# Kernel tuning notes

Hardware: AMD Instinct MI355X
Metric: run time of the kernel (lower is better)

The kernel has to match this reference:

```python
import jax, jax.numpy as jnp
import numpy as np

THRESHOLD = 0.3

def setup_inputs() -> dict:
    key = jax.random.key(0)
    ks = jax.random.split(key, 8)
    B, T, N, d = 4, 32, 1024, 2
    hd, od, hs, osz = 64, 64, 128, 2
    p = lambda k, sh: jax.random.normal(k, sh, jnp.float32) * 0.1
    return {
        "points": jax.random.uniform(ks[0], (B, T, N, d), jnp.float32),
        "W1": p(ks[1], (hd, d)),   "b1": jnp.zeros((hd,), jnp.float32),
        "W2": p(ks[2], (od, hd)),  "b2": jnp.zeros((od,), jnp.float32),
        "Wg": p(ks[3], (hd, od)),  "bg": jnp.zeros((hd,), jnp.float32),
        "Wih": p(ks[4], (3 * hs, hd)), "Whh": p(ks[5], (3 * hs, hs)),
        "bih": jnp.zeros((3 * hs,), jnp.float32), "bhh": jnp.zeros((3 * hs,), jnp.float32),
        "Wf": p(ks[6], (osz, hs)), "bf": jnp.zeros((osz,), jnp.float32),
    }

def _gcn_step(pts, W1, b1, W2, b2, Wg, bg):
    # pts: [N, d]. Torch detaches node features & adjacency (no grad to points).
    pts = jax.lax.stop_gradient(pts)
    dist = jnp.linalg.norm(pts[:, None, :] - pts[None, :, :], axis=2)  # [N,N]
    A = (dist < THRESHOLD).astype(pts.dtype)
    dinv = 1.0 / jnp.sqrt(A.sum(axis=1))          # rowsum >= 1 (self-loop)
    An = A * dinv[:, None] * dinv[None, :]        # D^{-1/2} A D^{-1/2}
    x = jax.nn.relu((An @ pts) @ W1.T + b1)       # [N, hd]
    x = jax.nn.relu((An @ x) @ W2.T + b2)         # [N, od]
    return x.mean(axis=0) @ Wg.T + bg             # [hd]

def reference(points, W1, b1, W2, b2, Wg, bg, Wih, Whh, bih, bhh, Wf, bf):
    # GCN per (batch, time): [B, T, hd]
    gcn = jax.vmap(jax.vmap(lambda p: _gcn_step(p, W1, b1, W2, b2, Wg, bg)))(points)
    H = Whh.shape[1]

    def gru_step(h, x):  # torch GRU gate order: r, z, n
        gi = x @ Wih.T + bih
        gh = h @ Whh.T + bhh
        ir, iz, inn = jnp.split(gi, 3)
        hr, hz, hn = jnp.split(gh, 3)
        r = jax.nn.sigmoid(ir + hr)
        z = jax.nn.sigmoid(iz + hz)
        n = jnp.tanh(inn + r * hn)
        h_new = (1.0 - z) * n + z * h
        return h_new, h_new

    h0 = jnp.zeros((H,), points.dtype)
    run = lambda xs: jax.lax.scan(gru_step, h0, xs)[1]   # [T, H]
    hs = jax.vmap(run)(gcn)                              # [B, T, H]
    y = hs @ Wf.T + bf                                   # [B, T, out]
    # torch: per-element gru_out.mean(dim=1, keepdim=True) on [1,T,out] -> [1,1,out], stacked -> [B,1,1,out]
    return y.mean(axis=1, keepdims=True)[:, :, None, :]
```

## Files before the change

kernel.cpp:

```cpp
#include <hip/hip_runtime.h>
#include <hip/hip_bf16.h>
#include <math.h>

#define N_PTS 1024
#define BT    128
typedef unsigned int u32;
typedef __attribute__((ext_vector_type(8))) short short8_t;
typedef __attribute__((ext_vector_type(4))) float f32x4;

__device__ __forceinline__ float bfi(u32 bits16) {
    union { u32 u; float f; } v; v.u = bits16 << 16; return v.f;
}
__device__ __forceinline__ unsigned short f2bf(float f) {
    union { float f; u32 u; } v; v.f = f;
    return (unsigned short)((v.u + 0x7FFFu + ((v.u >> 16) & 1u)) >> 16);
}
__device__ __forceinline__ float ldf(const void* p, int i, bool bf) {
    return bf ? bfi(((const unsigned short*)p)[i]) : ((const float*)p)[i];
}
__device__ __forceinline__ float2 ldp(const void* pbase, int j, bool bf) {
    if (bf) {
        u32 w = ((const u32*)pbase)[j];
        return make_float2(bfi(w & 0xFFFFu), bfi(w >> 16));
    }
    return ((const float2*)pbase)[j];
}
__device__ __forceinline__ bool detect_bf16(const void* pts, int tid, int* s_flag) {
    if (tid < 64) {
        u32 w = ((const u32*)pts)[tid];
        float v = bfi(w & 0xFFFFu);
        bool ok = (v >= 0.0f) && (v <= 1.0f);
        unsigned long long m = __ballot(ok);
        if (tid == 0) *s_flag = (m == 0xFFFFFFFFFFFFFFFFull) ? 1 : 0;
    }
    __syncthreads();
    return *s_flag != 0;
}
__device__ __forceinline__ bool is_nb(float px, float py, float qx, float qy) {
    float dx = px - qx, dy = py - qy;
    float d2 = __fadd_rn(__fmul_rn(dx, dx), __fmul_rn(dy, dy));
    return d2 < 0.09f;
}
__device__ __forceinline__ const void* pts_base(const void* pts, int bt, bool bf) {
    return bf ? (const void*)((const unsigned short*)pts + (size_t)bt * N_PTS * 2)
              : (const void*)((const float*)pts + (size_t)bt * N_PTS * 2);
}
__device__ __forceinline__ void gload16(const u32* g, u32* l) {
    __builtin_amdgcn_global_load_lds((const __attribute__((address_space(1))) u32*)g,
                                     (__attribute__((address_space(3))) u32*)l, 16, 0, 0);
}
__device__ __forceinline__ float rdlane(float v, int i) {
    return __int_as_float(__builtin_amdgcn_readlane(__float_as_int(v), i));
}
__device__ __forceinline__ float sigm_f(float x) {
    return __fdividef(1.0f, 1.0f + __expf(-x));
}
__device__ __forceinline__ float tanh_f(float x) {
    float e = __expf(2.0f * x);
    return 1.0f - __fdividef(2.0f, e + 1.0f);
}

__global__ __launch_bounds__(256) void k1_bm(const void* __restrict__ pts,
                                             float* __restrict__ dinv,
                                             float* __restrict__ gsum,
                                             u32* __restrict__ bm) {
    int blk = blockIdx.x, tid = threadIdx.x;
    int bt = blk >> 2, q = blk & 3;
    __shared__ float2 sp[N_PTS];
    __shared__ int s_flag;
    bool bf = detect_bf16(pts, tid, &s_flag);
    const void* pb = pts_base(pts, bt, bf);
    for (int j = tid; j < N_PTS; j += 256) sp[j] = ldp(pb, j, bf);
    if (blk < 32) gsum[blk * 256 + tid] = 0.0f;
    __syncthreads();
    int i = q * 256 + tid;
    float px = sp[i].x, py = sp[i].y;
    const float4* sp4 = (const float4*)sp;
    u32* bmrow = bm + (size_t)bt * 32768 + i;
    int cnt = 0;
    for (int c = 0; c < 32; c++) {
        u32 m = 0;
#pragma unroll
        for (int h = 0; h < 8; h++) {
            float4 s01 = sp4[c * 16 + 2 * h], s23 = sp4[c * 16 + 2 * h + 1];
            if (is_nb(px, py, s01.x, s01.y)) m |= 1u << (4 * h);
            if (is_nb(px, py, s01.z, s01.w)) m |= 1u << (4 * h + 1);
            if (is_nb(px, py, s23.x, s23.y)) m |= 1u << (4 * h + 2);
            if (is_nb(px, py, s23.z, s23.w)) m |= 1u << (4 * h + 3);
        }
        bmrow[c * 1024] = m;
        cnt += __popc(m);
    }
    dinv[bt * N_PTS + i] = 1.0f / sqrtf((float)cnt);
}

__global__ __launch_bounds__(256) void k2_x1v(const void* __restrict__ pts,
                                              const void* __restrict__ W1,
                                              const void* __restrict__ b1,
                                              const float* __restrict__ dinv,
                                              const u32* __restrict__ bm,
                                              u32* __restrict__ x1vB) {
    int blk = blockIdx.x, tid = threadIdx.x;
    int bt = blk >> 2, q = blk & 3;
    __shared__ float2 sud[N_PTS];
    __shared__ float2 sax[256];
    __shared__ float  sdl[256];
    __shared__ int s_flag;
    bool bf = detect_bf16(pts, tid, &s_flag);
    const void* pb = pts_base(pts, bt, bf);
    for (int j = tid; j < N_PTS; j += 256) {
        float2 p = ldp(pb, j, bf);
        float d = dinv[bt * N_PTS + j];
        sud[j] = make_float2(d * p.x, d * p.y);
    }
    __syncthreads();
    int i = q * 256 + tid;
    float ax = 0.f, ay = 0.f;
    const u32* bmr = bm + (size_t)bt * 32768 + i;
    for (int c = 0; c < 32; c++) {
        u32 m = bmr[c * 1024];
        const float4* uv = (const float4*)sud + c * 16;
#pragma unroll
        for (int h = 0; h < 16; h++) {
            float4 v = uv[h];
            bool b0 = (m >> (2 * h)) & 1u, b1_ = (m >> (2 * h + 1)) & 1u;
            ax += b0 ? v.x : 0.0f;  ay += b0 ? v.y : 0.0f;
            ax += b1_ ? v.z : 0.0f; ay += b1_ ? v.w : 0.0f;
        }
    }
    float di = dinv[bt * N_PTS + i];
    sax[tid] = make_float2(ax * di, ay * di);
    sdl[tid] = di;
    __syncthreads();
    int ch = tid & 63, wq = tid >> 6;
    float w0 = ldf(W1, 2 * ch, bf), w1v = ldf(W1, 2 * ch + 1, bf), bb = ldf(b1, ch, bf);
    for (int tt = 0; tt < 4; tt++) {
        u32 ow[8];
#pragma unroll
        for (int k2i = 0; k2i < 8; k2i++) {
            int lj = tt * 64 + wq * 16 + 2 * k2i;
            float2 a0 = sax[lj], a1 = sax[lj + 1];
            float v0 = sdl[lj]     * fmaxf(fmaf(w0, a0.x, fmaf(w1v, a0.y, bb)), 0.0f);
            float v1 = sdl[lj + 1] * fmaxf(fmaf(w0, a1.x, fmaf(w1v, a1.y, bb)), 0.0f);
            ow[k2i] = (u32)f2bf(v0) | ((u32)f2bf(v1) << 16);
        }
        u32* dst = x1vB + ((size_t)(bt * 16 + q * 4 + tt) * 64 + ch) * 36 + wq * 8;
        *(uint4*)dst = make_uint4(ow[0], ow[1], ow[2], ow[3]);
        *(uint4*)(dst + 4) = make_uint4(ow[4], ow[5], ow[6], ow[7]);
    }
}

__global__ __launch_bounds__(256) void k3_mfma(const void* __restrict__ pts,
                                               const void* __restrict__ W2,
                                               const void* __restrict__ b2,
                                               const float* __restrict__ dinv,
                                               const u32* __restrict__ bm,
                                               const u32* __restrict__ x1vB,
                                               float* __restrict__ gsum) {
    __shared__ u32 pool[15424];
    __shared__ int s_flag;
    float* poolf = (float*)pool;
    int tid = threadIdx.x, lane = tid & 63, w = tid >> 6;
    int l15 = lane & 15, quad = lane >> 4;
    int blk = blockIdx.x, bt = blk & 127, rowblk = blk >> 7;
    bool bf = detect_bf16(pts, tid, &s_flag);

    const u32* xg = x1vB + (size_t)bt * 36864;
    for (int it = w; it < 9; it += 4)
        gload16(xg + it * 256 + lane * 4, pool + 8192 + it * 256 + lane * 4);

    const u32* bg_ = bm + (size_t)bt * 32768 + rowblk * 256;
    for (int idx = tid; idx < 8192; idx += 256) {
        int c = idx >> 8, r = idx & 255;
        pool[idx] = bg_[c * 1024 + r];
    }
    unsigned short* W2B = (unsigned short*)(pool + 12800);
    for (int idx = tid; idx < 4096; idx += 256) {
        int o = idx >> 6, c = idx & 63;
        W2B[o * 72 + c] = f2bf(ldf(W2, idx, bf));
    }
    if (tid < 256) poolf[15104 + tid] = dinv[bt * N_PTS + rowblk * 256 + tid];
    if (tid < 64)  poolf[15360 + tid] = ldf(b2, tid, bf);

    f32x4 acc[4][4];
#pragma unroll
    for (int rf = 0; rf < 4; rf++)
#pragma unroll
        for (int nb = 0; nb < 4; nb++)
#pragma unroll
            for (int r = 0; r < 4; r++) acc[rf][nb][r] = 0.0f;

    for (int t = 0; t < 16; t++) {
        __syncthreads();
        if (t + 1 < 16) {
            u32* dst = pool + ((t & 1) ? 8192 : 10496);
            const u32* src = xg + (t + 1) * 2304;
            for (int it = w; it < 9; it += 4)
                gload16(src + it * 256 + lane * 4, dst + it * 256 + lane * 4);
        }
        const unsigned short* xf = (const unsigned short*)(pool + ((t & 1) ? 10496 : 8192));
#pragma unroll
        for (int ks = 0; ks < 2; ks++) {
            short8_t bq[4];
#pragma unroll
            for (int rf = 0; rf < 4; rf++) {
                u32 mw = pool[(2 * t + ks) * 256 + w * 64 + rf * 16 + l15];
                u32 by = (mw >> (quad * 8)) & 0xFFu;
                short8_t v;
#pragma unroll
                for (int i2 = 0; i2 < 8; i2++)
                    v[i2] = (by & (1u << i2)) ? (short)0x3F80 : (short)0;
                bq[rf] = v;
            }
#pragma unroll
            for (int nb = 0; nb < 4; nb++) {
                short8_t af = *(const short8_t*)(xf + (nb * 16 + l15) * 72 + ks * 32 + quad * 8);
#pragma unroll
                for (int rf = 0; rf < 4; rf++)
                    acc[rf][nb] = __builtin_amdgcn_mfma_f32_16x16x32_bf16(af, bq[rf], acc[rf][nb], 0, 0, 0);
            }
        }
    }
    __syncthreads();

    u32* dump = pool;
#pragma unroll
    for (int rf = 0; rf < 4; rf++) {
        int rn = w * 64 + rf * 16 + l15;
        float di = poolf[15104 + rn];
#pragma unroll
        for (int nb = 0; nb < 4; nb++) {
            u32 lo = (u32)f2bf(acc[rf][nb][0] * di) | ((u32)f2bf(acc[rf][nb][1] * di) << 16);
            u32 hi = (u32)f2bf(acc[rf][nb][2] * di) | ((u32)f2bf(acc[rf][nb][3] * di) << 16);
            u32* dst = dump + rn * 36 + nb * 8 + quad * 2;
            dst[0] = lo; dst[1] = hi;
        }
    }
    __syncthreads();
    f32x4 xacc[4][4];
#pragma unroll
    for (int ob = 0; ob < 4; ob++)
#pragma unroll
        for (int rf = 0; rf < 4; rf++)
#pragma unroll
            for (int r = 0; r < 4; r++) xacc[ob][rf][r] = 0.0f;
#pragma unroll
    for (int ks2 = 0; ks2 < 2; ks2++) {
        short8_t b2f[4];
#pragma unroll
        for (int rf = 0; rf < 4; rf++)
            b2f[rf] = *(const short8_t*)((const unsigned short*)dump +
                        (w * 64 + rf * 16 + l15) * 72 + ks2 * 32 + quad * 8);
#pragma unroll
        for (int ob = 0; ob < 4; ob++) {
            short8_t a2 = *(const short8_t*)(W2B + (ob * 16 + l15) * 72 + ks2 * 32 + quad * 8);
#pragma unroll
            for (int rf = 0; rf < 4; rf++)
                xacc[ob][rf] = __builtin_amdgcn_mfma_f32_16x16x32_bf16(a2, b2f[rf], xacc[ob][rf], 0, 0, 0);
        }
    }
#pragma unroll
    for (int ob = 0; ob < 4; ob++) {
#pragma unroll
        for (int r = 0; r < 4; r++) {
            int o = ob * 16 + quad * 4 + r;
            float bb = poolf[15360 + o];
            float s = 0.0f;
#pragma unroll
            for (int rf = 0; rf < 4; rf++) s += fmaxf(xacc[ob][rf][r] + bb, 0.0f);
            s += __shfl_down(s, 8, 16);
            s += __shfl_down(s, 4, 16);
            s += __shfl_down(s, 2, 16);
            s += __shfl_down(s, 1, 16);
            if (l15 == 0) atomicAdd(&gsum[bt * 64 + o], s);
        }
    }
}

__global__ __launch_bounds__(768, 1) void k4_all(const void* __restrict__ pts,
                                                 const void* __restrict__ Wg,
                                                 const void* __restrict__ bg,
                                                 const void* __restrict__ Wih,
                                                 const void* __restrict__ Whh,
                                                 const void* __restrict__ bih,
                                                 const void* __restrict__ bhh,
                                                 const void* __restrict__ Wf,
                                                 const void* __restrict__ bf_,
                                                 const float* __restrict__ gsum,
                                                 float* __restrict__ out) {
    int b = blockIdx.x, tid = threadIdx.x;
    __shared__ float s_gi[32 * 384];
    __shared__ float sWgT[64 * 65];
    __shared__ float s_gm[2048];
    __shared__ float s_x[2048];
    __shared__ float s_part[2][768];
    __shared__ float s_hm[128];
    __shared__ int s_flag;
    bool bf = detect_bf16(pts, tid, &s_flag);
    for (int idx = tid; idx < 4096; idx += 768) {
        int o = idx >> 6, k = idx & 63;
        sWgT[k * 65 + o] = ldf(Wg, idx, bf);
    }
    for (int idx = tid; idx < 2048; idx += 768)
        s_gm[idx] = gsum[(size_t)b * 2048 + idx] * (1.0f / 1024.0f);
    __syncthreads();
    for (int idx = tid; idx < 2048; idx += 768) {
        int t = idx >> 6, c = idx & 63;
        float s0 = ldf(bg, c, bf), s1 = 0.f, s2 = 0.f, s3 = 0.f;
        const float* gm = s_gm + t * 64;
#pragma unroll
        for (int k = 0; k < 64; k += 4) {
            s0 = fmaf(sWgT[k * 65 + c],       gm[k],     s0);
            s1 = fmaf(sWgT[(k + 1) * 65 + c], gm[k + 1], s1);
            s2 = fmaf(sWgT[(k + 2) * 65 + c], gm[k + 2], s2);
            s3 = fmaf(sWgT[(k + 3) * 65 + c], gm[k + 3], s3);
        }
        s_x[idx] = (s0 + s1) + (s2 + s3);
    }
    __syncthreads();
    int hi = (tid >= 384) ? 1 : 0;
    int r = tid - hi * 384;
    int lane = tid & 63;
    {
        float wv[64];
        if (bf) {
#pragma unroll
            for (int k = 0; k < 64; k++) wv[k] = bfi(((const unsigned short*)Wih)[r * 64 + k]);
        } else {
            const float4* wr = (const float4*)Wih + r * 16;
#pragma unroll
            for (int qq = 0; qq < 16; qq++) {
                float4 v = wr[qq];
                wv[4*qq] = v.x; wv[4*qq+1] = v.y; wv[4*qq+2] = v.z; wv[4*qq+3] = v.w;
            }
        }
        float br = ldf(bih, r, bf);
        for (int t = hi; t < 32; t += 2) {
            float xv = s_x[t * 64 + lane];
            float s0 = br, s1 = 0.f, s2 = 0.f, s3 = 0.f;
#pragma unroll
            for (int k = 0; k < 64; k += 4) {
                s0 = fmaf(wv[k],     rdlane(xv, k),     s0);
                s1 = fmaf(wv[k + 1], rdlane(xv, k + 1), s1);
                s2 = fmaf(wv[k + 2], rdlane(xv, k + 2), s2);
                s3 = fmaf(wv[k + 3], rdlane(xv, k + 3), s3);
            }
            s_gi[t * 384 + r] = (s0 + s1) + (s2 + s3);
        }
    }
    float wh2[64];
    {
        int koff = hi * 64;
        if (bf) {
#pragma unroll
            for (int k = 0; k < 64; k++)
                wh2[k] = bfi(((const unsigned short*)Whh)[r * 128 + koff + k]);
        } else {
            const float4* wr = (const float4*)Whh + (r * 128 + koff) / 4;
#pragma unroll
            for (int qq = 0; qq < 16; qq++) {
                float4 v = wr[qq];
                wh2[4*qq] = v.x; wh2[4*qq+1] = v.y; wh2[4*qq+2] = v.z; wh2[4*qq+3] = v.w;
            }
        }
    }
    float bhr = hi ? 0.0f : ldf(bhh, r, bf);
    int c = hi * 64 + lane;
    float hval = 0.0f;
    float hsum = 0.0f;
    __syncthreads();

    for (int t = 0; t < 32; t++) {
        float gi_r = s_gi[t * 384 + c];
        float gi_z = s_gi[t * 384 + 128 + c];
        float gi_n = s_gi[t * 384 + 256 + c];
        float s0 = bhr, s1 = 0.f, s2 = 0.f, s3 = 0.f;
#pragma unroll
        for (int k = 0; k < 64; k += 4) {
            s0 = fmaf(wh2[k],     rdlane(hval, k),     s0);
            s1 = fmaf(wh2[k + 1], rdlane(hval, k + 1), s1);
            s2 = fmaf(wh2[k + 2], rdlane(hval, k + 2), s2);
            s3 = fmaf(wh2[k + 3], rdlane(hval, k + 3), s3);
        }
        s_part[t & 1][tid] = (s0 + s1) + (s2 + s3);
        __syncthreads();
        const float* P = s_part[t & 1];
        float gr = gi_r + P[c]       + P[384 + c];
        float gz = gi_z + P[128 + c] + P[512 + c];
        float hn =        P[256 + c] + P[640 + c];
        float rr = sigm_f(gr);
        float z  = sigm_f(gz);
        float n  = tanh_f(fmaf(rr, hn, gi_n));
        hval = fmaf(z, hval - n, n);
        hsum += hval;
    }
    if (tid < 64) s_hm[tid] = hsum * (1.0f / 32.0f);
    else if (tid >= 384 && tid < 448) s_hm[64 + lane] = hsum * (1.0f / 32.0f);
    __syncthreads();
    if (tid < 128) {
        float hm = s_hm[tid];
        s_part[0][tid]       = ldf(Wf, tid, bf) * hm;
        s_part[0][128 + tid] = ldf(Wf, 128 + tid, bf) * hm;
    }
    __syncthreads();
    if (tid < 2) {
        float s = ldf(bf_, tid, bf);
        for (int k = 0; k < 128; k++) s += s_part[0][tid * 128 + k];
        out[b * 2 + tid] = s;
    }
}

extern "C" void kernel_launch(void* const* d_in, const int* in_sizes, int n_in,
                              void* d_out, int out_size, void* d_ws, size_t ws_size,
                              hipStream_t stream) {
    const void* pts = d_in[0];
    const void* W1  = d_in[1];
    const void* b1  = d_in[2];
    const void* W2  = d_in[3];
    const void* b2  = d_in[4];
    const void* Wg  = d_in[5];
    const void* bg  = d_in[6];
    const void* Wih = d_in[7];
    const void* Whh = d_in[8];
    const void* bih = d_in[9];
    const void* bhh = d_in[10];
    const void* Wf  = d_in[11];
    const void* bf_ = d_in[12];

    float* dinv = (float*)d_ws;
    float* gsum = dinv + (size_t)BT * N_PTS;
    u32*   bm   = (u32*)(gsum + BT * 64);
    u32*   x1vB = bm + (size_t)BT * 32768;

    k1_bm  <<<512, 256, 0, stream>>>(pts, dinv, gsum, bm);
    k2_x1v <<<512, 256, 0, stream>>>(pts, W1, b1, dinv, bm, x1vB);
    k3_mfma<<<512, 256, 0, stream>>>(pts, W2, b2, dinv, bm, x1vB, gsum);
    k4_all <<<4, 768, 0, stream>>>(pts, Wg, bg, Wih, Whh, bih, bhh, Wf, bf_,
                                   gsum, (float*)d_out);
}
```

Baseline: 242.2 us.

## Split GRU input projection into a separate 128-block kernel before the scan

The tail kernel, which ran on only 4 blocks, computed the Wg projection and the Wih input-gate projection for all 32 timesteps serially before starting the recurrent scan. That work now runs in a new kernel with one block per (batch, time) pair, writing the gate inputs to workspace that reuses the x1vB buffer. The scan kernel then bulk-loads those precomputed gate inputs into shared memory. This spreads the non-recurrent work across many CUs, at the cost of an extra kernel launch and a global-memory round trip.

```diff
diff --git a/kernel.cpp b/kernel.cpp
--- a/kernel.cpp
+++ b/kernel.cpp
@@ -277,77 +277,95 @@
     }
 }
 
-__global__ __launch_bounds__(768, 1) void k4_all(const void* __restrict__ pts,
+__global__ __launch_bounds__(384, 1) void k4a_gi(const void* __restrict__ pts,
                                                  const void* __restrict__ Wg,
                                                  const void* __restrict__ bg,
                                                  const void* __restrict__ Wih,
-                                                 const void* __restrict__ Whh,
                                                  const void* __restrict__ bih,
-                                                 const void* __restrict__ bhh,
-                                                 const void* __restrict__ Wf,
-                                                 const void* __restrict__ bf_,
                                                  const float* __restrict__ gsum,
-                                                 float* __restrict__ out) {
+                                                 float* __restrict__ gi_ws) {
+    int blk = blockIdx.x, tid = threadIdx.x;
+    __shared__ float s_gm[64];
+    __shared__ float s_x[64];
+    __shared__ int s_flag;
+    bool bf = detect_bf16(pts, tid, &s_flag);
+    if (tid < 64) s_gm[tid] = gsum[(size_t)blk * 64 + tid] * (1.0f / 1024.0f);
+    int r = tid;
+    float wv[64];
+    if (bf) {
+#pragma unroll
+        for (int k = 0; k < 64; k++) wv[k] = bfi(((const unsigned short*)Wih)[r * 64 + k]);
+    } else {
+        const float4* wr = (const float4*)Wih + r * 16;
+#pragma unroll
+        for (int qq = 0; qq < 16; qq++) {
+            float4 v = wr[qq];
+            wv[4*qq] = v.x; wv[4*qq+1] = v.y; wv[4*qq+2] = v.z; wv[4*qq+3] = v.w;
+        }
+    }
+    float br = ldf(bih, r, bf);
+    float wg[64];
+    if (tid < 64) {
+        if (bf) {
+#pragma unroll
+            for (int k = 0; k < 64; k++) wg[k] = bfi(((const unsigned short*)Wg)[tid * 64 + k]);
+        } else {
+            const float4* wr = (const float4*)Wg + tid * 16;
+#pragma unroll
+            for (int qq = 0; qq < 16; qq++) {
+                float4 v = wr[qq];
+                wg[4*qq] = v.x; wg[4*qq+1] = v.y; wg[4*qq+2] = v.z; wg[4*qq+3] = v.w;
+            }
+        }
+    }
+    __syncthreads();
+    if (tid < 64) {
+        float gmv = s_gm[tid];
+        float s0 = ldf(bg, tid, bf), s1 = 0.f, s2 = 0.f, s3 = 0.f;
+#pragma unroll
+        for (int k = 0; k < 64; k += 4) {
+            s0 = fmaf(wg[k],     rdlane(gmv, k),     s0);
+            s1 = fmaf(wg[k + 1], rdlane(gmv, k + 1), s1);
+            s2 = fmaf(wg[k + 2], rdlane(gmv, k + 2), s2);
+            s3 = fmaf(wg[k + 3], rdlane(gmv, k + 3), s3);
+        }
+        s_x[tid] = (s0 + s1) + (s2 + s3);
+    }
+    __syncthreads();
+    float xv = s_x[tid & 63];
+    float s0 = br, s1 = 0.f, s2 = 0.f, s3 = 0.f;
+#pragma unroll
+    for (int k = 0; k < 64; k += 4) {
+        s0 = fmaf(wv[k],     rdlane(xv, k),     s0);
+        s1 = fmaf(wv[k + 1], rdlane(xv, k + 1), s1);
+        s2 = fmaf(wv[k + 2], rdlane(xv, k + 2), s2);
+        s3 = fmaf(wv[k + 3], rdlane(xv, k + 3), s3);
+    }
+    gi_ws[(size_t)blk * 384 + r] = (s0 + s1) + (s2 + s3);
+}
+
+__global__ __launch_bounds__(768, 1) void k4b_scan(const void* __restrict__ pts,
+                                                   const void* __restrict__ Whh,
+                                                   const void* __restrict__ bhh,
+                                                   const void* __restrict__ Wf,
+                                                   const void* __restrict__ bf_,
+                                                   const float* __restrict__ gi_ws,
+                                                   float* __restrict__ out) {
     int b = blockIdx.x, tid = threadIdx.x;
-    __shared__ float s_gi[32 * 384];
-    __shared__ float sWgT[64 * 65];
-    __shared__ float s_gm[2048];
-    __shared__ float s_x[2048];
+    __shared__ float s_gi[12288];
     __shared__ float s_part[2][768];
     __shared__ float s_hm[128];
     __shared__ int s_flag;
     bool bf = detect_bf16(pts, tid, &s_flag);
-    for (int idx = tid; idx < 4096; idx += 768) {
-        int o = idx >> 6, k = idx & 63;
-        sWgT[k * 65 + o] = ldf(Wg, idx, bf);
-    }
-    for (int idx = tid; idx < 2048; idx += 768)
-        s_gm[idx] = gsum[(size_t)b * 2048 + idx] * (1.0f / 1024.0f);
-    __syncthreads();
-    for (int idx = tid; idx < 2048; idx += 768) {
-        int t = idx >> 6, c = idx & 63;
-        float s0 = ldf(bg, c, bf), s1 = 0.f, s2 = 0.f, s3 = 0.f;
-        const float* gm = s_gm + t * 64;
-#pragma unroll
-        for (int k = 0; k < 64; k += 4) {
-            s0 = fmaf(sWgT[k * 65 + c],       gm[k],     s0);
-            s1 = fmaf(sWgT[(k + 1) * 65 + c], gm[k + 1], s1);
-            s2 = fmaf(sWgT[(k + 2) * 65 + c], gm[k + 2], s2);
-            s3 = fmaf(sWgT[(k + 3) * 65 + c], gm[k + 3], s3);
-        }
-        s_x[idx] = (s0 + s1) + (s2 + s3);
-    }
-    __syncthreads();
+    const u32* gi_g = (const u32*)gi_ws + (size_t)b * 12288;
+    u32* s_gi_u = (u32*)s_gi;
+#pragma unroll
+    for (int j = 0; j < 4; j++)
+        gload16(gi_g + j * 3072 + tid * 4, s_gi_u + j * 3072 + tid * 4);
+
     int hi = (tid >= 384) ? 1 : 0;
     int r = tid - hi * 384;
     int lane = tid & 63;
-    {
-        float wv[64];
-        if (bf) {
-#pragma unroll
-            for (int k = 0; k < 64; k++) wv[k] = bfi(((const unsigned short*)Wih)[r * 64 + k]);
-        } else {
-            const float4* wr = (const float4*)Wih + r * 16;
-#pragma unroll
-            for (int qq = 0; qq < 16; qq++) {
-                float4 v = wr[qq];
-                wv[4*qq] = v.x; wv[4*qq+1] = v.y; wv[4*qq+2] = v.z; wv[4*qq+3] = v.w;
-            }
-        }
-        float br = ldf(bih, r, bf);
-        for (int t = hi; t < 32; t += 2) {
-            float xv = s_x[t * 64 + lane];
-            float s0 = br, s1 = 0.f, s2 = 0.f, s3 = 0.f;
-#pragma unroll
-            for (int k = 0; k < 64; k += 4) {
-                s0 = fmaf(wv[k],     rdlane(xv, k),     s0);
-                s1 = fmaf(wv[k + 1], rdlane(xv, k + 1), s1);
-                s2 = fmaf(wv[k + 2], rdlane(xv, k + 2), s2);
-                s3 = fmaf(wv[k + 3], rdlane(xv, k + 3), s3);
-            }
-            s_gi[t * 384 + r] = (s0 + s1) + (s2 + s3);
-        }
-    }
     float wh2[64];
     {
         int koff = hi * 64;
@@ -431,10 +449,11 @@
     float* gsum = dinv + (size_t)BT * N_PTS;
     u32*   bm   = (u32*)(gsum + BT * 64);
     u32*   x1vB = bm + (size_t)BT * 32768;
+    float* gi_ws = (float*)x1vB;
 
     k1_bm  <<<512, 256, 0, stream>>>(pts, dinv, gsum, bm);
     k2_x1v <<<512, 256, 0, stream>>>(pts, W1, b1, dinv, bm, x1vB);
     k3_mfma<<<512, 256, 0, stream>>>(pts, W2, b2, dinv, bm, x1vB, gsum);
-    k4_all <<<4, 768, 0, stream>>>(pts, Wg, bg, Wih, Whh, bih, bhh, Wf, bf_,
-                                   gsum, (float*)d_out);
-}
+    k4a_gi <<<128, 384, 0, stream>>>(pts, Wg, bg, Wih, bih, gsum, gi_ws);
+    k4b_scan<<<4, 768, 0, stream>>>(pts, Whh, bhh, Wf, bf_, gi_ws, (float*)d_out);
+}
```

Result: faster. 233.6 us (-3.6%).
